# Performance work log

Measured on AMD Instinct MI355X. Metric: run time of the kernel, lower is better.

The kernel has to match this reference:

```python
import jax, jax.numpy as jnp
import numpy as np

EPS = 1e-5
QB = 127.0  # int8 activation quantization bound

def rmsnorm(x):
    # SimpleRMSNorm: x / rms(x), no learned scale
    return x * jax.lax.rsqrt(jnp.mean(x * x, axis=-1, keepdims=True) + EPS)

def activation_quant(x):
    # per-token absmax int8 quant-dequant
    scale = QB / jnp.clip(jnp.max(jnp.abs(x), axis=-1, keepdims=True), EPS)
    return jnp.clip(jnp.round(x * scale), -QB - 1, QB) / scale

def weight_quant(w):
    # per-tensor ternary quant-dequant (BitNet b1.58)
    scale = 1.0 / jnp.clip(jnp.mean(jnp.abs(w)), EPS)
    return jnp.clip(jnp.round(w * scale), -1.0, 1.0) / scale

def ste(x, q):
    # straight-through estimator: forward uses q, gradient flows to x
    return x + jax.lax.stop_gradient(q - x)

def bitlinear(x, w, b):
    xn = rmsnorm(x)
    xq = ste(xn, activation_quant(xn))
    wq = ste(w, weight_quant(w))
    # x: [b, s, d_in], w: [d_out, d_in] -> [b, s, d_out]
    return jnp.einsum('bsd,od->bso', xq, wq) + b

def setup_inputs() -> dict:
    key = jax.random.key(0)
    k1, k2, k3, k4, k5 = jax.random.split(key, 5)
    dim, inner = 1024, 4096
    x = jax.random.normal(k1, (4, 4096, dim), dtype=jnp.float32)
    w1 = jax.random.normal(k2, (inner, dim), dtype=jnp.float32) * (dim ** -0.5)
    b1 = jax.random.normal(k3, (inner,), dtype=jnp.float32) * 0.02
    w2 = jax.random.normal(k4, (dim, inner), dtype=jnp.float32) * (inner ** -0.5)
    b2 = jax.random.normal(k5, (dim,), dtype=jnp.float32) * 0.02
    return {"x": x, "w1": w1, "b1": b1, "w2": w2, "b2": b2}

def reference(x, w1, b1, w2, b2):
    h = jax.nn.gelu(bitlinear(x, w1, b1), approximate=False)  # torch nn.GELU default = exact erf
    # dropout p=0.0 is identity; post_act_ln disabled
    return bitlinear(h, w2, b2)
```

## Files before the change

### kernel.cpp

```cpp
#include <hip/hip_runtime.h>
#include <hip/hip_bf16.h>

#define TOK   16384
#define DIM   1024
#define INNER 4096
#define EPSF  1e-5f

typedef int v4i __attribute__((ext_vector_type(4)));

static __device__ __forceinline__ float bf2f(unsigned short u) {
    return __uint_as_float(((unsigned)u) << 16);
}
static __device__ __forceinline__ unsigned short f2bf(float f) {
    unsigned u = __float_as_uint(f);
    return (unsigned short)((u + 0x7fffu + ((u >> 16) & 1u)) >> 16);
}

static __device__ __forceinline__ float waveSum(float v) {
#pragma unroll
    for (int o = 32; o > 0; o >>= 1) v += __shfl_down(v, o, 64);
    return v;
}
static __device__ __forceinline__ float waveMax(float v) {
#pragma unroll
    for (int o = 32; o > 0; o >>= 1) v = fmaxf(v, __shfl_down(v, o, 64));
    return v;
}

__global__ void absmean_k(const float* __restrict__ w, int n4, float* __restrict__ acc) {
    int idx = blockIdx.x * blockDim.x + threadIdx.x;
    int stride = gridDim.x * blockDim.x;
    const float4* w4 = (const float4*)w;
    float s = 0.f;
    for (int i = idx; i < n4; i += stride) {
        float4 v = w4[i];
        s += fabsf(v.x) + fabsf(v.y) + fabsf(v.z) + fabsf(v.w);
    }
    __shared__ float sp[4];
    int wv = threadIdx.x >> 6, lane = threadIdx.x & 63;
    s = waveSum(s);
    if (lane == 0) sp[wv] = s;
    __syncthreads();
    if (threadIdx.x == 0) atomicAdd(acc, sp[0] + sp[1] + sp[2] + sp[3]);
}

__global__ void wquant_k(const float* __restrict__ w, int n,
                         const float* __restrict__ acc, float* __restrict__ wscale,
                         char* __restrict__ wq) {
    float mean = *acc / (float)n;
    float cl = fmaxf(mean, EPSF);
    float s = 1.f / cl;
    if (blockIdx.x == 0 && threadIdx.x == 0) *wscale = cl;
    int idx = blockIdx.x * blockDim.x + threadIdx.x;
    int stride = gridDim.x * blockDim.x;
    int n4 = n >> 2;
    const float4* w4 = (const float4*)w;
    unsigned* q4 = (unsigned*)wq;
    for (int i = idx; i < n4; i += stride) {
        float4 v = w4[i];
        float e[4] = {v.x, v.y, v.z, v.w};
        unsigned packed = 0;
#pragma unroll
        for (int j = 0; j < 4; j++) {
            float r = rintf(e[j] * s);
            r = fminf(fmaxf(r, -1.f), 1.f);
            packed |= ((unsigned)((int)r & 0xff)) << (8 * j);
        }
        q4[i] = packed;
    }
}

template <int D, int VPT>
__global__ void actquant_f32_k(const float* __restrict__ X, char* __restrict__ Q,
                               float* __restrict__ rs_out) {
    int token = blockIdx.x;
    int t = threadIdx.x;
    const float4* xp = (const float4*)(X + (long)token * D);
    float vals[VPT];
    float ss = 0.f, am = 0.f;
#pragma unroll
    for (int j = 0; j < VPT / 4; j++) {
        float4 v = xp[t * (VPT / 4) + j];
        vals[4 * j] = v.x; vals[4 * j + 1] = v.y; vals[4 * j + 2] = v.z; vals[4 * j + 3] = v.w;
        ss += v.x * v.x + v.y * v.y + v.z * v.z + v.w * v.w;
        am = fmaxf(am, fmaxf(fmaxf(fabsf(v.x), fabsf(v.y)), fmaxf(fabsf(v.z), fabsf(v.w))));
    }
    __shared__ float sp[8];
    __shared__ float bc[2];
    int wv = t >> 6, lane = t & 63;
    float S = waveSum(ss);
    float M = waveMax(am);
    if (lane == 0) { sp[wv] = S; sp[4 + wv] = M; }
    __syncthreads();
    if (t == 0) {
        float Sa = sp[0] + sp[1] + sp[2] + sp[3];
        float Ma = fmaxf(fmaxf(sp[4], sp[5]), fmaxf(sp[6], sp[7]));
        float rinv = rsqrtf(Sa * (1.f / (float)D) + EPSF);
        float amn = Ma * rinv;
        float scale = 127.f / fmaxf(amn, EPSF);
        rs_out[token] = 1.f / scale;
        bc[0] = rinv; bc[1] = scale;
    }
    __syncthreads();
    float rinv = bc[0], scale = bc[1];
    unsigned outw[VPT / 4];
#pragma unroll
    for (int j = 0; j < VPT; j++) {
        float r = rintf((vals[j] * rinv) * scale);
        r = fminf(fmaxf(r, -128.f), 127.f);
        unsigned qi = (unsigned)((int)r & 0xff) << (8 * (j & 3));
        if ((j & 3) == 0) outw[j / 4] = qi; else outw[j / 4] |= qi;
    }
    unsigned* qp = (unsigned*)(Q + (long)token * D);
#pragma unroll
    for (int j = 0; j < VPT / 4; j++) qp[t * (VPT / 4) + j] = outw[j];
}

template <int D, int VPT>
__global__ void actquant_bf16_k(const unsigned short* __restrict__ X, char* __restrict__ Q,
                                float* __restrict__ rs_out) {
    int token = blockIdx.x;
    int t = threadIdx.x;
    const unsigned* x2 = (const unsigned*)(X + (long)token * D);
    float vals[VPT];
    float ss = 0.f, am = 0.f;
#pragma unroll
    for (int j = 0; j < VPT / 2; j++) {
        unsigned v = x2[t * (VPT / 2) + j];
        float f0 = bf2f((unsigned short)(v & 0xffff));
        float f1 = bf2f((unsigned short)(v >> 16));
        vals[2 * j] = f0; vals[2 * j + 1] = f1;
        ss += f0 * f0 + f1 * f1;
        am = fmaxf(am, fmaxf(fabsf(f0), fabsf(f1)));
    }
    __shared__ float sp[8];
    __shared__ float bc[2];
    int wv = t >> 6, lane = t & 63;
    float S = waveSum(ss);
    float M = waveMax(am);
    if (lane == 0) { sp[wv] = S; sp[4 + wv] = M; }
    __syncthreads();
    if (t == 0) {
        float Sa = sp[0] + sp[1] + sp[2] + sp[3];
        float Ma = fmaxf(fmaxf(sp[4], sp[5]), fmaxf(sp[6], sp[7]));
        float rinv = rsqrtf(Sa * (1.f / (float)D) + EPSF);
        float amn = Ma * rinv;
        float scale = 127.f / fmaxf(amn, EPSF);
        rs_out[token] = 1.f / scale;
        bc[0] = rinv; bc[1] = scale;
    }
    __syncthreads();
    float rinv = bc[0], scale = bc[1];
    unsigned outw[VPT / 4];
#pragma unroll
    for (int j = 0; j < VPT; j++) {
        float r = rintf((vals[j] * rinv) * scale);
        r = fminf(fmaxf(r, -128.f), 127.f);
        unsigned qi = (unsigned)((int)r & 0xff) << (8 * (j & 3));
        if ((j & 3) == 0) outw[j / 4] = qi; else outw[j / 4] |= qi;
    }
    unsigned* qp = (unsigned*)(Q + (long)token * D);
#pragma unroll
    for (int j = 0; j < VPT / 4; j++) qp[t * (VPT / 4) + j] = outw[j];
}

#define LDR 80
template <int DO_GELU, int OUT_F32>
__global__ __launch_bounds__(256) void gemm_i8_k(
    const char* __restrict__ A, const char* __restrict__ Bw,
    const float* __restrict__ rs, const float* __restrict__ wscale_p,
    const float* __restrict__ bias, void* __restrict__ outp,
    int M, int N, int K) {
    __shared__ char As[128 * LDR];
    __shared__ char Bs[128 * LDR];
    int t = threadIdx.x;
    int n0 = blockIdx.x * 128, m0 = blockIdx.y * 128;
    int wv = t >> 6, lane = t & 63, lm = lane & 15, q = lane >> 4;
    int wrow = (wv >> 1) * 64, wcol = (wv & 1) * 64;

    int r = t >> 2, c = t & 3;
    const uint4* Ap0 = (const uint4*)(A + (long)(m0 + r) * K + c * 16);
    const uint4* Ap1 = (const uint4*)(A + (long)(m0 + r + 64) * K + c * 16);
    const uint4* Bp0 = (const uint4*)(Bw + (long)(n0 + r) * K + c * 16);
    const uint4* Bp1 = (const uint4*)(Bw + (long)(n0 + r + 64) * K + c * 16);
    uint4* Asw0 = (uint4*)(As + r * LDR + c * 16);
    uint4* Asw1 = (uint4*)(As + (r + 64) * LDR + c * 16);
    uint4* Bsw0 = (uint4*)(Bs + r * LDR + c * 16);
    uint4* Bsw1 = (uint4*)(Bs + (r + 64) * LDR + c * 16);

    v4i acc[4][4] = {};
    const char* arow[4];
    const char* brow[4];
#pragma unroll
    for (int i = 0; i < 4; i++) {
        arow[i] = As + (wrow + i * 16 + lm) * LDR + q * 16;
        brow[i] = Bs + (wcol + i * 16 + lm) * LDR + q * 16;
    }

    for (int k0 = 0; k0 < K; k0 += 64) {
        int kc = k0 >> 4;
        uint4 a0 = Ap0[kc], a1 = Ap1[kc], b0 = Bp0[kc], b1 = Bp1[kc];
        __syncthreads();
        *Asw0 = a0; *Asw1 = a1; *Bsw0 = b0; *Bsw1 = b1;
        __syncthreads();
        v4i a[4], b[4];
#pragma unroll
        for (int i = 0; i < 4; i++) { a[i] = *(const v4i*)arow[i]; b[i] = *(const v4i*)brow[i]; }
#pragma unroll
        for (int i = 0; i < 4; i++)
#pragma unroll
            for (int j = 0; j < 4; j++)
                acc[i][j] = __builtin_amdgcn_mfma_i32_16x16x64_i8(a[i], b[j], acc[i][j], 0, 0, 0);
    }

    float wsc = *wscale_p;
#pragma unroll
    for (int i = 0; i < 4; i++) {
        int mg = m0 + wrow + i * 16 + q * 4;
        float fs[4];
#pragma unroll
        for (int rr = 0; rr < 4; rr++) fs[rr] = rs[mg + rr] * wsc;
#pragma unroll
        for (int j = 0; j < 4; j++) {
            int ng = n0 + wcol + j * 16 + lm;
            float bv = bias[ng];
#pragma unroll
            for (int rr = 0; rr < 4; rr++) {
                float v = (float)acc[i][j][rr] * fs[rr] + bv;
                if (DO_GELU) v = 0.5f * v * (1.f + erff(v * 0.70710678118654752f));
                long idx = (long)(mg + rr) * N + ng;
                if (OUT_F32) ((float*)outp)[idx] = v;
                else ((unsigned short*)outp)[idx] = f2bf(v);
            }
        }
    }
}

extern "C" void kernel_launch(void* const* d_in, const int* in_sizes, int n_in,
                              void* d_out, int out_size, void* d_ws, size_t ws_size,
                              hipStream_t stream) {
    const float* x  = (const float*)d_in[0];
    const float* w1 = (const float*)d_in[1];
    const float* b1 = (const float*)d_in[2];
    const float* w2 = (const float*)d_in[3];
    const float* b2 = (const float*)d_in[4];
    float* out = (float*)d_out;

    char* ws = (char*)d_ws;
    float* acc1 = (float*)(ws + 0);
    float* acc2 = (float*)(ws + 4);
    float* wsc1 = (float*)(ws + 8);
    float* wsc2 = (float*)(ws + 12);
    size_t off = 256;
    char* w1q = ws + off; off += (size_t)INNER * DIM;
    char* w2q = ws + off; off += (size_t)INNER * DIM;
    char* xq1 = ws + off; off += (size_t)TOK * DIM;
    float* rs1 = (float*)(ws + off); off += (size_t)TOK * 4;
    char* xq2 = ws + off; off += (size_t)TOK * INNER;
    float* rs2 = (float*)(ws + off); off += (size_t)TOK * 4;
    unsigned short* h = (unsigned short*)(ws + off);

    hipMemsetAsync(d_ws, 0, 16, stream);

    int nw = INNER * DIM;
    absmean_k<<<1024, 256, 0, stream>>>(w1, nw / 4, acc1);
    absmean_k<<<1024, 256, 0, stream>>>(w2, nw / 4, acc2);
    wquant_k<<<2048, 256, 0, stream>>>(w1, nw, acc1, wsc1, w1q);
    wquant_k<<<2048, 256, 0, stream>>>(w2, nw, acc2, wsc2, w2q);

    actquant_f32_k<DIM, 4><<<TOK, 256, 0, stream>>>(x, xq1, rs1);
    gemm_i8_k<1, 0><<<dim3(INNER / 128, TOK / 128), 256, 0, stream>>>(
        xq1, w1q, rs1, wsc1, b1, (void*)h, TOK, INNER, DIM);
    actquant_bf16_k<INNER, 16><<<TOK, 256, 0, stream>>>(h, xq2, rs2);
    gemm_i8_k<0, 1><<<dim3(DIM / 128, TOK / 128), 256, 0, stream>>>(
        xq2, w2q, rs2, wsc2, b2, (void*)out, TOK, DIM, INNER);
}
```

Before: 470.4 us.

## Load int8 GEMM tiles directly into LDS with XOR-swizzled layout

Measured after the change: 465.0 us. No clear change (-1.2%).

```diff
diff --git a/kernel.cpp b/kernel.cpp
--- a/kernel.cpp
+++ b/kernel.cpp
@@ -7,6 +7,12 @@
 #define EPSF  1e-5f
 
 typedef int v4i __attribute__((ext_vector_type(4)));
+
+static __device__ __forceinline__ void async_copy16(const char* g, char* l) {
+    __builtin_amdgcn_global_load_lds(
+        (const __attribute__((address_space(1))) unsigned int*)g,
+        (__attribute__((address_space(3))) unsigned int*)l, 16, 0, 0);
+}
 
 static __device__ __forceinline__ float bf2f(unsigned short u) {
     return __uint_as_float(((unsigned)u) << 16);
@@ -164,53 +170,52 @@
     for (int j = 0; j < VPT / 4; j++) qp[t * (VPT / 4) + j] = outw[j];
 }
 
-#define LDR 80
 template <int DO_GELU, int OUT_F32>
 __global__ __launch_bounds__(256) void gemm_i8_k(
     const char* __restrict__ A, const char* __restrict__ Bw,
     const float* __restrict__ rs, const float* __restrict__ wscale_p,
     const float* __restrict__ bias, void* __restrict__ outp,
     int M, int N, int K) {
-    __shared__ char As[128 * LDR];
-    __shared__ char Bs[128 * LDR];
+    __shared__ char As[8192];
+    __shared__ char Bs[8192];
     int t = threadIdx.x;
     int n0 = blockIdx.x * 128, m0 = blockIdx.y * 128;
     int wv = t >> 6, lane = t & 63, lm = lane & 15, q = lane >> 4;
     int wrow = (wv >> 1) * 64, wcol = (wv & 1) * 64;
 
-    int r = t >> 2, c = t & 3;
-    const uint4* Ap0 = (const uint4*)(A + (long)(m0 + r) * K + c * 16);
-    const uint4* Ap1 = (const uint4*)(A + (long)(m0 + r + 64) * K + c * 16);
-    const uint4* Bp0 = (const uint4*)(Bw + (long)(n0 + r) * K + c * 16);
-    const uint4* Bp1 = (const uint4*)(Bw + (long)(n0 + r + 64) * K + c * 16);
-    uint4* Asw0 = (uint4*)(As + r * LDR + c * 16);
-    uint4* Asw1 = (uint4*)(As + (r + 64) * LDR + c * 16);
-    uint4* Bsw0 = (uint4*)(Bs + r * LDR + c * 16);
-    uint4* Bsw1 = (uint4*)(Bs + (r + 64) * LDR + c * 16);
+    int r = t >> 2;
+    int csrc = (t & 3) ^ (r & 3);
+    const char* Ap = A + (long)(m0 + r) * K + csrc * 16;
+    const char* Bp = Bw + (long)(n0 + r) * K + csrc * 16;
+    long rowoff = (long)64 * K;
 
     v4i acc[4][4] = {};
-    const char* arow[4];
-    const char* brow[4];
+    const v4i* As4 = (const v4i*)As;
+    const v4i* Bs4 = (const v4i*)Bs;
+    int aidx[4], bidx[4];
 #pragma unroll
     for (int i = 0; i < 4; i++) {
-        arow[i] = As + (wrow + i * 16 + lm) * LDR + q * 16;
-        brow[i] = Bs + (wcol + i * 16 + lm) * LDR + q * 16;
+        int ml = wrow + i * 16 + lm;
+        aidx[i] = ml * 4 + (q ^ (ml & 3));
+        int nl = wcol + i * 16 + lm;
+        bidx[i] = nl * 4 + (q ^ (nl & 3));
     }
 
     for (int k0 = 0; k0 < K; k0 += 64) {
-        int kc = k0 >> 4;
-        uint4 a0 = Ap0[kc], a1 = Ap1[kc], b0 = Bp0[kc], b1 = Bp1[kc];
-        __syncthreads();
-        *Asw0 = a0; *Asw1 = a1; *Bsw0 = b0; *Bsw1 = b1;
+        async_copy16(Ap + k0,          As + t * 16);
+        async_copy16(Ap + rowoff + k0, As + 4096 + t * 16);
+        async_copy16(Bp + k0,          Bs + t * 16);
+        async_copy16(Bp + rowoff + k0, Bs + 4096 + t * 16);
         __syncthreads();
         v4i a[4], b[4];
 #pragma unroll
-        for (int i = 0; i < 4; i++) { a[i] = *(const v4i*)arow[i]; b[i] = *(const v4i*)brow[i]; }
+        for (int i = 0; i < 4; i++) { a[i] = As4[aidx[i]]; b[i] = Bs4[bidx[i]]; }
 #pragma unroll
         for (int i = 0; i < 4; i++)
 #pragma unroll
             for (int j = 0; j < 4; j++)
                 acc[i][j] = __builtin_amdgcn_mfma_i32_16x16x64_i8(a[i], b[j], acc[i][j], 0, 0, 0);
+        __syncthreads();
     }
 
     float wsc = *wscale_p;
```
